# Kernel optimization log

Measured on AMD Instinct MI355X. Metric: run time of the kernel, lower is better.

## Reference

```python
import jax, jax.numpy as jnp
import numpy as np

EPS = 1e-08

def setup_inputs() -> dict:
    key = jax.random.key(0)
    x = jax.random.normal(key, (8192,), dtype=jnp.float32)
    return {"x": x}

def reference(x):
    xf = x.reshape(-1)
    n = xf.shape[0]
    min_x = jnp.min(xf)
    # shift so all values are non-negative only when min is negative (matches torch branch)
    xf = jnp.where(min_x < 0, xf - min_x, xf)
    mu = jnp.mean(xf) + EPS
    # explicit O(n^2) pairwise abs-diff sum, same math as the torch module
    sum_diff = jnp.sum(jnp.abs(xf[None, :] - xf[:, None]))
    gini = sum_diff / (2.0 * (n * n) * mu)
    return gini
```

## Files before the change

kernel.cpp:

```cpp
#include <hip/hip_runtime.h>


#define EPS 1e-8f

__global__ void __launch_bounds__(256) gini_pair_partial(
    const float* __restrict__ x, float* __restrict__ partials, int n) {
    __shared__ __align__(16) float sm[8192];
    const int nchunks = n >> 2;
    {
        const float4* xv = (const float4*)x;
        float4* smv = (float4*)sm;
        for (int i = threadIdx.x; i < nchunks; i += 256) smv[i] = xv[i];
    }
    __syncthreads();

    int g     = blockIdx.x * 256 + threadIdx.x;
    int group = g >> 7;
    int seg   = g & 127;
    int row0  = group * 8;

    float acc0 = 0.f, acc1 = 0.f, acc2 = 0.f, acc3 = 0.f;
    float acc4 = 0.f, acc5 = 0.f, acc6 = 0.f, acc7 = 0.f;
    if (row0 + 7 < n) {
        float r0 = sm[row0 + 0], r1 = sm[row0 + 1];
        float r2 = sm[row0 + 2], r3 = sm[row0 + 3];
        float r4 = sm[row0 + 4], r5 = sm[row0 + 5];
        float r6 = sm[row0 + 6], r7 = sm[row0 + 7];
        const float4* sm4 = (const float4*)sm;
        #pragma unroll 4
        for (int c = seg; c < nchunks; c += 128) {
            float4 v = sm4[c];
            acc0 += (fabsf(r0 - v.x) + fabsf(r0 - v.y)) + (fabsf(r0 - v.z) + fabsf(r0 - v.w));
            acc1 += (fabsf(r1 - v.x) + fabsf(r1 - v.y)) + (fabsf(r1 - v.z) + fabsf(r1 - v.w));
            acc2 += (fabsf(r2 - v.x) + fabsf(r2 - v.y)) + (fabsf(r2 - v.z) + fabsf(r2 - v.w));
            acc3 += (fabsf(r3 - v.x) + fabsf(r3 - v.y)) + (fabsf(r3 - v.z) + fabsf(r3 - v.w));
            acc4 += (fabsf(r4 - v.x) + fabsf(r4 - v.y)) + (fabsf(r4 - v.z) + fabsf(r4 - v.w));
            acc5 += (fabsf(r5 - v.x) + fabsf(r5 - v.y)) + (fabsf(r5 - v.z) + fabsf(r5 - v.w));
            acc6 += (fabsf(r6 - v.x) + fabsf(r6 - v.y)) + (fabsf(r6 - v.z) + fabsf(r6 - v.w));
            acc7 += (fabsf(r7 - v.x) + fabsf(r7 - v.y)) + (fabsf(r7 - v.z) + fabsf(r7 - v.w));
        }
    }
    float acc = ((acc0 + acc1) + (acc2 + acc3)) + ((acc4 + acc5) + (acc6 + acc7));

    #pragma unroll
    for (int off = 32; off > 0; off >>= 1) acc += __shfl_down(acc, off, 64);
    __shared__ float wsum[4];
    int wave = threadIdx.x >> 6;
    if ((threadIdx.x & 63) == 0) wsum[wave] = acc;
    __syncthreads();
    if (threadIdx.x == 0)
        partials[blockIdx.x] = (wsum[0] + wsum[1]) + (wsum[2] + wsum[3]);
}

__global__ void __launch_bounds__(256) gini_finalize(
    const float* __restrict__ x, const float* __restrict__ partials,
    int nblocks, float* __restrict__ out, int n) {
    float lmin = 3.4e38f, lsum = 0.0f, psum = 0.0f;
    for (int i = threadIdx.x; i < n; i += 256) {
        float v = x[i];
        lmin = fminf(lmin, v);
        lsum += v;
    }
    for (int i = threadIdx.x; i < nblocks; i += 256) psum += partials[i];

    #pragma unroll
    for (int off = 32; off > 0; off >>= 1) {
        lmin = fminf(lmin, __shfl_down(lmin, off, 64));
        lsum += __shfl_down(lsum, off, 64);
        psum += __shfl_down(psum, off, 64);
    }
    __shared__ float smin[4], ssum[4], spsum[4];
    int wave = threadIdx.x >> 6;
    if ((threadIdx.x & 63) == 0) {
        smin[wave] = lmin; ssum[wave] = lsum; spsum[wave] = psum;
    }
    __syncthreads();
    if (threadIdx.x == 0) {
        float mn  = fminf(fminf(smin[0], smin[1]), fminf(smin[2], smin[3]));
        float sum = (ssum[0] + ssum[1]) + (ssum[2] + ssum[3]);
        float sd  = (spsum[0] + spsum[1]) + (spsum[2] + spsum[3]);
        float shifted_sum = (mn < 0.0f) ? (sum - (float)n * mn) : sum;
        float mu = shifted_sum / (float)n + EPS;
        out[0] = sd / (2.0f * (float)n * (float)n * mu);
    }
}

extern "C" void kernel_launch(void* const* d_in, const int* in_sizes, int n_in,
                              void* d_out, int out_size, void* d_ws, size_t ws_size,
                              hipStream_t stream) {
    const float* x = (const float*)d_in[0];
    float* out = (float*)d_out;
    float* partials = (float*)d_ws;
    int n = in_sizes[0];

    int nblocks = (n * 16 + 255) / 256;
    gini_pair_partial<<<nblocks, 256, 0, stream>>>(x, partials, n);
    gini_finalize<<<1, 256, 0, stream>>>(x, partials, nblocks, out, n);
}
```

Baseline: 64.51 us.

## Fuse pair-sum and finalize kernels via cooperative grid sync

Merges the partial-sum kernel and the single-block finalize kernel into one cooperative launch. Blocks publish partials with release stores, then a grid-wide sync lets block 0 gather them and compute min, mean and the final Gini. This drops the second kernel launch and the re-read of x from global memory. In exchange it pays for a grid barrier and needs all 512 blocks to be co-resident, which the cooperative launch requires.

```diff
diff --git a/kernel.cpp b/kernel.cpp
--- a/kernel.cpp
+++ b/kernel.cpp
@@ -1,10 +1,14 @@
 #include <hip/hip_runtime.h>
+#include <hip/hip_cooperative_groups.h>
+
+namespace cg = cooperative_groups;
 
 
 #define EPS 1e-8f
 
-__global__ void __launch_bounds__(256) gini_pair_partial(
-    const float* __restrict__ x, float* __restrict__ partials, int n) {
+__global__ void __launch_bounds__(256) gini_fused(
+    const float* __restrict__ x, float* __restrict__ partials,
+    float* __restrict__ out, int n) {
     __shared__ __align__(16) float sm[8192];
     const int nchunks = n >> 2;
     {
@@ -42,46 +46,53 @@
     }
     float acc = ((acc0 + acc1) + (acc2 + acc3)) + ((acc4 + acc5) + (acc6 + acc7));
 
+    float lmin = 3.4e38f, lsum = 0.0f;
+    if (blockIdx.x == 0) {
+        for (int i = threadIdx.x; i < n; i += 256) {
+            float v = sm[i];
+            lmin = fminf(lmin, v);
+            lsum += v;
+        }
+    }
+
     #pragma unroll
     for (int off = 32; off > 0; off >>= 1) acc += __shfl_down(acc, off, 64);
     __shared__ float wsum[4];
     int wave = threadIdx.x >> 6;
     if ((threadIdx.x & 63) == 0) wsum[wave] = acc;
     __syncthreads();
-    if (threadIdx.x == 0)
-        partials[blockIdx.x] = (wsum[0] + wsum[1]) + (wsum[2] + wsum[3]);
-}
+    if (threadIdx.x == 0) {
+        float bs = (wsum[0] + wsum[1]) + (wsum[2] + wsum[3]);
+        __hip_atomic_store(&partials[blockIdx.x], bs, __ATOMIC_RELEASE,
+                           __HIP_MEMORY_SCOPE_AGENT);
+    }
 
-__global__ void __launch_bounds__(256) gini_finalize(
-    const float* __restrict__ x, const float* __restrict__ partials,
-    int nblocks, float* __restrict__ out, int n) {
-    float lmin = 3.4e38f, lsum = 0.0f, psum = 0.0f;
-    for (int i = threadIdx.x; i < n; i += 256) {
-        float v = x[i];
-        lmin = fminf(lmin, v);
-        lsum += v;
-    }
-    for (int i = threadIdx.x; i < nblocks; i += 256) psum += partials[i];
+    cg::this_grid().sync();
 
-    #pragma unroll
-    for (int off = 32; off > 0; off >>= 1) {
-        lmin = fminf(lmin, __shfl_down(lmin, off, 64));
-        lsum += __shfl_down(lsum, off, 64);
-        psum += __shfl_down(psum, off, 64);
-    }
-    __shared__ float smin[4], ssum[4], spsum[4];
-    int wave = threadIdx.x >> 6;
-    if ((threadIdx.x & 63) == 0) {
-        smin[wave] = lmin; ssum[wave] = lsum; spsum[wave] = psum;
-    }
-    __syncthreads();
-    if (threadIdx.x == 0) {
-        float mn  = fminf(fminf(smin[0], smin[1]), fminf(smin[2], smin[3]));
-        float sum = (ssum[0] + ssum[1]) + (ssum[2] + ssum[3]);
-        float sd  = (spsum[0] + spsum[1]) + (spsum[2] + spsum[3]);
-        float shifted_sum = (mn < 0.0f) ? (sum - (float)n * mn) : sum;
-        float mu = shifted_sum / (float)n + EPS;
-        out[0] = sd / (2.0f * (float)n * (float)n * mu);
+    if (blockIdx.x == 0) {
+        float psum = 0.0f;
+        for (unsigned i = threadIdx.x; i < gridDim.x; i += 256)
+            psum += __hip_atomic_load(&partials[i], __ATOMIC_ACQUIRE,
+                                      __HIP_MEMORY_SCOPE_AGENT);
+        #pragma unroll
+        for (int off = 32; off > 0; off >>= 1) {
+            lmin = fminf(lmin, __shfl_down(lmin, off, 64));
+            lsum += __shfl_down(lsum, off, 64);
+            psum += __shfl_down(psum, off, 64);
+        }
+        __shared__ float smin[4], ssum[4], spsum[4];
+        if ((threadIdx.x & 63) == 0) {
+            smin[wave] = lmin; ssum[wave] = lsum; spsum[wave] = psum;
+        }
+        __syncthreads();
+        if (threadIdx.x == 0) {
+            float mn  = fminf(fminf(smin[0], smin[1]), fminf(smin[2], smin[3]));
+            float sum = (ssum[0] + ssum[1]) + (ssum[2] + ssum[3]);
+            float sd  = (spsum[0] + spsum[1]) + (spsum[2] + spsum[3]);
+            float shifted_sum = (mn < 0.0f) ? (sum - (float)n * mn) : sum;
+            float mu = shifted_sum / (float)n + EPS;
+            out[0] = sd / (2.0f * (float)n * (float)n * mu);
+        }
     }
 }
 
@@ -94,6 +105,7 @@
     int n = in_sizes[0];
 
     int nblocks = (n * 16 + 255) / 256;
-    gini_pair_partial<<<nblocks, 256, 0, stream>>>(x, partials, n);
-    gini_finalize<<<1, 256, 0, stream>>>(x, partials, nblocks, out, n);
+    void* args[] = {(void*)&x, (void*)&partials, (void*)&out, (void*)&n};
+    hipLaunchCooperativeKernel((void*)gini_fused, dim3(nblocks), dim3(256),
+                               args, 0, stream);
 }
```

New measurement: 135.5 us. 110% more time.

## Exploit pairwise symmetry to compute only upper-triangle absolute differences

Applied to the files above, without the earlier changes.

Each block now processes a row group and its mirror group, comparing each row only against columns from its own group onward, so roughly half the pairwise differences are evaluated. Intra-group lower-triangle pairs are subtracted and the finalize doubles the sum. This targets the O(n^2) arithmetic cost, at the price of a less regular per-thread loop and a small per-block correction term.

```diff
diff --git a/kernel.cpp b/kernel.cpp
--- a/kernel.cpp
+++ b/kernel.cpp
@@ -14,39 +14,64 @@
     }
     __syncthreads();
 
-    int g     = blockIdx.x * 256 + threadIdx.x;
-    int group = g >> 7;
-    int seg   = g & 127;
-    int row0  = group * 8;
+    const int ngroups = n >> 3;
+    const int gA = blockIdx.x;
+    const int gB = ngroups - 1 - gA;
+    const int t  = threadIdx.x;
 
-    float acc0 = 0.f, acc1 = 0.f, acc2 = 0.f, acc3 = 0.f;
-    float acc4 = 0.f, acc5 = 0.f, acc6 = 0.f, acc7 = 0.f;
-    if (row0 + 7 < n) {
-        float r0 = sm[row0 + 0], r1 = sm[row0 + 1];
-        float r2 = sm[row0 + 2], r3 = sm[row0 + 3];
-        float r4 = sm[row0 + 4], r5 = sm[row0 + 5];
-        float r6 = sm[row0 + 6], r7 = sm[row0 + 7];
-        const float4* sm4 = (const float4*)sm;
-        #pragma unroll 4
-        for (int c = seg; c < nchunks; c += 128) {
-            float4 v = sm4[c];
-            acc0 += (fabsf(r0 - v.x) + fabsf(r0 - v.y)) + (fabsf(r0 - v.z) + fabsf(r0 - v.w));
-            acc1 += (fabsf(r1 - v.x) + fabsf(r1 - v.y)) + (fabsf(r1 - v.z) + fabsf(r1 - v.w));
-            acc2 += (fabsf(r2 - v.x) + fabsf(r2 - v.y)) + (fabsf(r2 - v.z) + fabsf(r2 - v.w));
-            acc3 += (fabsf(r3 - v.x) + fabsf(r3 - v.y)) + (fabsf(r3 - v.z) + fabsf(r3 - v.w));
-            acc4 += (fabsf(r4 - v.x) + fabsf(r4 - v.y)) + (fabsf(r4 - v.z) + fabsf(r4 - v.w));
-            acc5 += (fabsf(r5 - v.x) + fabsf(r5 - v.y)) + (fabsf(r5 - v.z) + fabsf(r5 - v.w));
-            acc6 += (fabsf(r6 - v.x) + fabsf(r6 - v.y)) + (fabsf(r6 - v.z) + fabsf(r6 - v.w));
-            acc7 += (fabsf(r7 - v.x) + fabsf(r7 - v.y)) + (fabsf(r7 - v.z) + fabsf(r7 - v.w));
-        }
+    float rA[8], rB[8];
+    #pragma unroll
+    for (int i = 0; i < 8; ++i) {
+        rA[i] = sm[gA * 8 + i];
+        rB[i] = sm[gB * 8 + i];
     }
-    float acc = ((acc0 + acc1) + (acc2 + acc3)) + ((acc4 + acc5) + (acc6 + acc7));
+
+    float acc[8];
+    #pragma unroll
+    for (int i = 0; i < 8; ++i) acc[i] = 0.0f;
+
+    const float4* sm4 = (const float4*)sm;
+
+    for (int c = 2 * gA + t; c < nchunks; c += 256) {
+        float4 v = sm4[c];
+        #pragma unroll
+        for (int i = 0; i < 8; ++i)
+            acc[i] += (fabsf(rA[i] - v.x) + fabsf(rA[i] - v.y)) +
+                      (fabsf(rA[i] - v.z) + fabsf(rA[i] - v.w));
+    }
+    for (int c = 2 * gB + t; c < nchunks; c += 256) {
+        float4 v = sm4[c];
+        #pragma unroll
+        for (int i = 0; i < 8; ++i)
+            acc[i] += (fabsf(rB[i] - v.x) + fabsf(rB[i] - v.y)) +
+                      (fabsf(rB[i] - v.z) + fabsf(rB[i] - v.w));
+    }
+
+    float a = ((acc[0] + acc[1]) + (acc[2] + acc[3])) +
+              ((acc[4] + acc[5]) + (acc[6] + acc[7]));
+
+    if (t == 0) {
+        float s = 0.0f;
+        #pragma unroll
+        for (int i = 0; i < 8; ++i)
+            #pragma unroll
+            for (int j = i + 1; j < 8; ++j) s += fabsf(rA[i] - rA[j]);
+        a -= s;
+    }
+    if (t == 1) {
+        float s = 0.0f;
+        #pragma unroll
+        for (int i = 0; i < 8; ++i)
+            #pragma unroll
+            for (int j = i + 1; j < 8; ++j) s += fabsf(rB[i] - rB[j]);
+        a -= s;
+    }
 
     #pragma unroll
-    for (int off = 32; off > 0; off >>= 1) acc += __shfl_down(acc, off, 64);
+    for (int off = 32; off > 0; off >>= 1) a += __shfl_down(a, off, 64);
     __shared__ float wsum[4];
     int wave = threadIdx.x >> 6;
-    if ((threadIdx.x & 63) == 0) wsum[wave] = acc;
+    if ((threadIdx.x & 63) == 0) wsum[wave] = a;
     __syncthreads();
     if (threadIdx.x == 0)
         partials[blockIdx.x] = (wsum[0] + wsum[1]) + (wsum[2] + wsum[3]);
@@ -78,7 +103,7 @@
     if (threadIdx.x == 0) {
         float mn  = fminf(fminf(smin[0], smin[1]), fminf(smin[2], smin[3]));
         float sum = (ssum[0] + ssum[1]) + (ssum[2] + ssum[3]);
-        float sd  = (spsum[0] + spsum[1]) + (spsum[2] + spsum[3]);
+        float sd  = 2.0f * ((spsum[0] + spsum[1]) + (spsum[2] + spsum[3]));
         float shifted_sum = (mn < 0.0f) ? (sum - (float)n * mn) : sum;
         float mu = shifted_sum / (float)n + EPS;
         out[0] = sd / (2.0f * (float)n * (float)n * mu);
@@ -93,7 +118,8 @@
     float* partials = (float*)d_ws;
     int n = in_sizes[0];
 
-    int nblocks = (n * 16 + 255) / 256;
+    int ngroups = n >> 3;
+    int nblocks = ngroups >> 1;
     gini_pair_partial<<<nblocks, 256, 0, stream>>>(x, partials, n);
     gini_finalize<<<1, 256, 0, stream>>>(x, partials, nblocks, out, n);
 }
```

Measured after the change: 62.82 us. 2.6% less time.
